# Kernel optimization log

Measured on AMD Instinct MI355X. Metric: run time of the kernel, lower is better.

## Reference

```python
import jax, jax.numpy as jnp
import numpy as np

B = 16384      # rays
H = 128        # field hidden dim


def setup_inputs() -> dict:
    key = jax.random.key(0)
    ks = jax.random.split(key, 8)
    origins = jax.random.normal(ks[0], (B, 3), dtype=jnp.float32)
    directions = jax.random.normal(ks[1], (B, 3), dtype=jnp.float32)
    directions = directions / jnp.linalg.norm(directions, axis=-1, keepdims=True)
    # Field: simple MLP 3 -> H -> H -> 4 (rgb + sigma)
    W1 = jax.random.normal(ks[2], (3, H), dtype=jnp.float32) * (1.0 / np.sqrt(3.0))
    b1 = jnp.zeros((H,), dtype=jnp.float32)
    W2 = jax.random.normal(ks[3], (H, H), dtype=jnp.float32) * (1.0 / np.sqrt(H))
    b2 = jnp.zeros((H,), dtype=jnp.float32)
    W3 = jax.random.normal(ks[4], (H, 4), dtype=jnp.float32) * (1.0 / np.sqrt(H))
    b3 = jnp.zeros((4,), dtype=jnp.float32)
    return {"origins": origins, "directions": directions,
            "W1": W1, "b1": b1, "W2": W2, "b2": b2, "W3": W3, "b3": b3,
            "near": 2, "far": 6, "num_samples": 64}


def _field(x, W1, b1, W2, b2, W3, b3):
    h = jax.nn.relu(x @ W1 + b1)
    h = jax.nn.relu(h @ W2 + b2)
    return h @ W3 + b3


def reference(origins, directions, W1, b1, W2, b2, W3, b3, near, far, num_samples):
    near = jnp.float32(near)
    far = jnp.float32(far)
    # 1. generate_samples: segment boundaries + midpoints along each ray
    depths = jnp.linspace(near, far, num_samples + 1)            # [S+1]
    midpoints = 0.5 * (depths[:-1] + depths[1:])                 # [S]
    # [B, S, 3] = origin + t * direction
    locs = origins[:, None, :] + midpoints[None, :, None] * directions[:, None, :]
    # 2. evaluate field
    f = _field(locs.reshape(-1, 3), W1, b1, W2, b2, W3, b3)
    f = f.reshape(origins.shape[0], num_samples, 4)
    # NOTE: source overwrites the sigmoid'd colors with raw outputs (faithful)
    colors = f[..., :3]                                          # [B, S, 3]
    sigma = f[..., 3]                                            # [B, S]
    # 3. alpha values
    delta = depths[1:] - depths[:-1]                             # [S]
    alphas = 1.0 - jnp.exp(-sigma * delta[None, :])              # [B, S]
    # 4. alpha compositing (black background)
    ones = jnp.ones_like(alphas[:, :1])
    transmittance = jnp.cumprod(jnp.concatenate([ones, 1.0 - alphas], axis=1), axis=1)[:, :-1]
    weights = alphas * transmittance                             # [B, S]
    radiance = jnp.sum(weights[..., None] * colors, axis=1)      # [B, 3]
    return radiance
```

## Files before the change

### kernel.cpp

```cpp
#include <hip/hip_runtime.h>


typedef _Float16 f16;
typedef __attribute__((ext_vector_type(2))) _Float16 h2v;
typedef __attribute__((ext_vector_type(8))) _Float16 half8;
typedef __attribute__((ext_vector_type(4))) float floatx4;

#define H 128
#define NS 64

static __device__ __forceinline__ h2v pkrtz(float a, float b) {
  return __builtin_bit_cast(h2v, __builtin_amdgcn_cvt_pkrtz(a, b));
}

__global__ void nerf_setup(const float* __restrict__ W2, const float* __restrict__ W3,
                           const float* __restrict__ b2,
                           f16* __restrict__ wsW2, f16* __restrict__ wsW3,
                           f16* __restrict__ wsB2) {
  int t = blockIdx.x * blockDim.x + threadIdx.x;
  if (t < 8192) {
    int j2 = t & 3, lane = (t >> 2) & 63, mt = (t >> 8) & 7, ks = t >> 11;
    int l16 = lane & 15;
    int k = ks * 32 + ((lane >> 4) * 8) + 2 * j2;
    int n = 32 * (l16 >> 2) + mt * 4 + (l16 & 3);
    wsW2[2 * t]     = (f16)W2[k * H + n];
    wsW2[2 * t + 1] = (f16)W2[(k + 1) * H + n];
  } else if (t < 9216) {
    int u = t - 8192;
    int j2 = u & 3, lane = (u >> 2) & 63, ks = u >> 8;
    int c = lane & 15;
    int k3 = 32 * (lane >> 4) + ks * 8 + 2 * j2;
    wsW3[2 * u]     = (c < 4) ? (f16)W3[k3 * 4 + c]       : (f16)0.0f;
    wsW3[2 * u + 1] = (c < 4) ? (f16)W3[(k3 + 1) * 4 + c] : (f16)0.0f;
  } else if (t < 9344) {
    int i = t - 9216;
    wsB2[i] = (f16)b2[i];
  }
}

__global__ __launch_bounds__(256, 2) void nerf_main(
    const float* __restrict__ origins, const float* __restrict__ dirs,
    const float* __restrict__ W1, const float* __restrict__ b1,
    const float* __restrict__ b3,
    const f16* __restrict__ wsW2, const f16* __restrict__ wsW3,
    const f16* __restrict__ wsB2,
    float* __restrict__ out)
{
  __shared__ __align__(16) f16   popd[4][2][H];
  __shared__ __align__(16) float f_lds[4][64][4];

  const int t = threadIdx.x;
  const int w = t >> 6, lane = t & 63, quad = lane >> 4, l16 = lane & 15;
  const float delta = 4.0f / NS;
  const int ray = blockIdx.x * 4 + w;

  {
    const float o0 = origins[ray*3], o1 = origins[ray*3+1], o2 = origins[ray*3+2];
    const float d0 = dirs[ray*3],    d1 = dirs[ray*3+1],    d2 = dirs[ray*3+2];
    const int k0 = lane * 2;
    const float2 wr0 = *(const float2*)&W1[0*H + k0];
    const float2 wr1 = *(const float2*)&W1[1*H + k0];
    const float2 wr2 = *(const float2*)&W1[2*H + k0];
    const float2 bb  = *(const float2*)&b1[k0];
    float poa = fmaf(o2, wr2.x, fmaf(o1, wr1.x, fmaf(o0, wr0.x, bb.x)));
    float pob = fmaf(o2, wr2.y, fmaf(o1, wr1.y, fmaf(o0, wr0.y, bb.y)));
    float pda = fmaf(d2, wr2.x, fmaf(d1, wr1.x, d0 * wr0.x));
    float pdb = fmaf(d2, wr2.y, fmaf(d1, wr1.y, d0 * wr0.y));
    h2v po2; po2[0] = (f16)poa; po2[1] = (f16)pob;
    h2v pd2; pd2[0] = (f16)pda; pd2[1] = (f16)pdb;
    *(h2v*)&popd[w][0][k0] = po2;
    *(h2v*)&popd[w][1][k0] = pd2;
  }

  half8 m8[4];
  #pragma unroll
  for (int tr = 0; tr < 4; ++tr)
    m8[tr] = (half8)(f16)(2.0f + (tr*16 + l16 + 0.5f) * delta);

  floatx4 acc[8][4];
  #pragma unroll
  for (int mt = 0; mt < 8; ++mt)
    #pragma unroll
    for (int tr = 0; tr < 4; ++tr) acc[mt][tr] = (floatx4)(0.0f);

  const half8* w2f = (const half8*)wsW2;
  const half8 z8 = (half8)(f16)0.0f;
  half8 awA[8], awB[8];
  #pragma unroll
  for (int mt = 0; mt < 8; ++mt) awA[mt] = w2f[mt*64 + lane];

  #pragma unroll
  for (int ks = 0; ks < 4; ++ks) {
    half8* cur = (ks & 1) ? awB : awA;
    half8* nxt = (ks & 1) ? awA : awB;
    if (ks < 3) {
      #pragma unroll
      for (int mt = 0; mt < 8; ++mt) nxt[mt] = w2f[((ks+1)*8 + mt)*64 + lane];
    }
    const half8 po8 = *(const half8*)&popd[w][0][ks*32 + quad*8];
    const half8 pd8 = *(const half8*)&popd[w][1][ks*32 + quad*8];
    #pragma unroll
    for (int tr = 0; tr < 4; ++tr) {
      half8 hb = pd8 * m8[tr] + po8;
      hb = __builtin_elementwise_max(hb, z8);
      #pragma unroll
      for (int mt = 0; mt < 8; ++mt)
        acc[mt][tr] = __builtin_amdgcn_mfma_f32_16x16x32_f16(cur[mt], hb, acc[mt][tr], 0, 0, 0);
    }
  }

  h2v bk0[8], bk1[8];
  {
    const uint2* bp = (const uint2*)wsB2;
    #pragma unroll
    for (int mt = 0; mt < 8; ++mt) {
      uint2 u = bp[quad * 8 + mt];
      bk0[mt] = __builtin_bit_cast(h2v, u.x);
      bk1[mt] = __builtin_bit_cast(h2v, u.y);
    }
  }
  const half8* w3f = (const half8*)wsW3;
  half8 w3[4];
  #pragma unroll
  for (int ks = 0; ks < 4; ++ks) w3[ks] = w3f[ks*64 + lane];

  const h2v z2 = (h2v)(f16)0.0f;
  floatx4 acc3[4];
  #pragma unroll
  for (int tr = 0; tr < 4; ++tr) {
    acc3[tr] = (floatx4)(0.0f);
    #pragma unroll
    for (int ks = 0; ks < 4; ++ks) {
      const int mt0 = 2*ks, mt1 = 2*ks + 1;
      h2v c0 = __builtin_elementwise_max((h2v)(pkrtz(acc[mt0][tr][0], acc[mt0][tr][1]) + bk0[mt0]), z2);
      h2v c1 = __builtin_elementwise_max((h2v)(pkrtz(acc[mt0][tr][2], acc[mt0][tr][3]) + bk1[mt0]), z2);
      h2v c2 = __builtin_elementwise_max((h2v)(pkrtz(acc[mt1][tr][0], acc[mt1][tr][1]) + bk0[mt1]), z2);
      h2v c3 = __builtin_elementwise_max((h2v)(pkrtz(acc[mt1][tr][2], acc[mt1][tr][3]) + bk1[mt1]), z2);
      half8 b = { c0[0], c0[1], c1[0], c1[1], c2[0], c2[1], c3[0], c3[1] };
      acc3[tr] = __builtin_amdgcn_mfma_f32_16x16x32_f16(w3[ks], b, acc3[tr], 0, 0, 0);
    }
  }

  if (quad == 0) {
    #pragma unroll
    for (int tr = 0; tr < 4; ++tr) {
      float4 fv;
      fv.x = acc3[tr][0] + b3[0];
      fv.y = acc3[tr][1] + b3[1];
      fv.z = acc3[tr][2] + b3[2];
      fv.w = acc3[tr][3] + b3[3];
      *(float4*)&f_lds[w][tr*16 + l16][0] = fv;
    }
  }

  {
    const float4 fv = *(const float4*)&f_lds[w][lane][0];
    const float sigma = fv.w;
    const float alpha = 1.0f - __expf(-sigma * delta);
    float S = sigma;
    #pragma unroll
    for (int off = 1; off < 64; off <<= 1) {
      float u = __shfl_up(S, off);
      if (lane >= off) S += u;
    }
    const float T  = __expf(-delta * (S - sigma));
    const float wt = alpha * T;
    float cr = wt * fv.x, cg = wt * fv.y, cb = wt * fv.z;
    #pragma unroll
    for (int off = 32; off > 0; off >>= 1) {
      cr += __shfl_down(cr, off);
      cg += __shfl_down(cg, off);
      cb += __shfl_down(cb, off);
    }
    if (lane == 0) {
      out[ray*3+0] = cr; out[ray*3+1] = cg; out[ray*3+2] = cb;
    }
  }
}

extern "C" void kernel_launch(void* const* d_in, const int* in_sizes, int n_in,
                              void* d_out, int out_size, void* d_ws, size_t ws_size,
                              hipStream_t stream) {
  const float* origins = (const float*)d_in[0];
  const float* dirs    = (const float*)d_in[1];
  const float* W1      = (const float*)d_in[2];
  const float* b1      = (const float*)d_in[3];
  const float* W2      = (const float*)d_in[4];
  const float* b2      = (const float*)d_in[5];
  const float* W3      = (const float*)d_in[6];
  const float* b3      = (const float*)d_in[7];
  float* out = (float*)d_out;

  f16* wsW2 = (f16*)d_ws;
  f16* wsW3 = wsW2 + 16384;
  f16* wsB2 = wsW3 + 2048;

  nerf_setup<<<37, 256, 0, stream>>>(W2, W3, b2, wsW2, wsW3, wsB2);
  nerf_main<<<16384 / 4, 256, 0, stream>>>(
      origins, dirs, W1, b1, b3, wsW2, wsW3, wsB2, out);
}
```

Before: 107.9 us.

## Split each ray across two waves to cut registers and raise occupancy

```diff
diff --git a/kernel.cpp b/kernel.cpp
--- a/kernel.cpp
+++ b/kernel.cpp
@@ -38,7 +38,7 @@
   }
 }
 
-__global__ __launch_bounds__(256, 2) void nerf_main(
+__global__ __launch_bounds__(256, 3) void nerf_main(
     const float* __restrict__ origins, const float* __restrict__ dirs,
     const float* __restrict__ W1, const float* __restrict__ b1,
     const float* __restrict__ b3,
@@ -47,12 +47,14 @@
     float* __restrict__ out)
 {
   __shared__ __align__(16) f16   popd[4][2][H];
-  __shared__ __align__(16) float f_lds[4][64][4];
+  __shared__ __align__(16) float f_lds[2][64][4];
 
   const int t = threadIdx.x;
   const int w = t >> 6, lane = t & 63, quad = lane >> 4, l16 = lane & 15;
+  const int rayw  = w >> 1;
+  const int ray   = blockIdx.x * 2 + rayw;
+  const int shalf = (w & 1) * 32;
   const float delta = 4.0f / NS;
-  const int ray = blockIdx.x * 4 + w;
 
   {
     const float o0 = origins[ray*3], o1 = origins[ray*3+1], o2 = origins[ray*3+2];
@@ -72,40 +74,34 @@
     *(h2v*)&popd[w][1][k0] = pd2;
   }
 
-  half8 m8[4];
+  half8 m8[2];
   #pragma unroll
-  for (int tr = 0; tr < 4; ++tr)
-    m8[tr] = (half8)(f16)(2.0f + (tr*16 + l16 + 0.5f) * delta);
+  for (int tr = 0; tr < 2; ++tr)
+    m8[tr] = (half8)(f16)(2.0f + (shalf + tr*16 + l16 + 0.5f) * delta);
 
-  floatx4 acc[8][4];
+  floatx4 acc[8][2];
   #pragma unroll
-  for (int mt = 0; mt < 8; ++mt)
-    #pragma unroll
-    for (int tr = 0; tr < 4; ++tr) acc[mt][tr] = (floatx4)(0.0f);
+  for (int mt = 0; mt < 8; ++mt) {
+    acc[mt][0] = (floatx4)(0.0f);
+    acc[mt][1] = (floatx4)(0.0f);
+  }
 
   const half8* w2f = (const half8*)wsW2;
   const half8 z8 = (half8)(f16)0.0f;
-  half8 awA[8], awB[8];
-  #pragma unroll
-  for (int mt = 0; mt < 8; ++mt) awA[mt] = w2f[mt*64 + lane];
-
   #pragma unroll
   for (int ks = 0; ks < 4; ++ks) {
-    half8* cur = (ks & 1) ? awB : awA;
-    half8* nxt = (ks & 1) ? awA : awB;
-    if (ks < 3) {
-      #pragma unroll
-      for (int mt = 0; mt < 8; ++mt) nxt[mt] = w2f[((ks+1)*8 + mt)*64 + lane];
-    }
+    half8 aw[8];
+    #pragma unroll
+    for (int mt = 0; mt < 8; ++mt) aw[mt] = w2f[(ks*8 + mt)*64 + lane];
     const half8 po8 = *(const half8*)&popd[w][0][ks*32 + quad*8];
     const half8 pd8 = *(const half8*)&popd[w][1][ks*32 + quad*8];
     #pragma unroll
-    for (int tr = 0; tr < 4; ++tr) {
+    for (int tr = 0; tr < 2; ++tr) {
       half8 hb = pd8 * m8[tr] + po8;
       hb = __builtin_elementwise_max(hb, z8);
       #pragma unroll
       for (int mt = 0; mt < 8; ++mt)
-        acc[mt][tr] = __builtin_amdgcn_mfma_f32_16x16x32_f16(cur[mt], hb, acc[mt][tr], 0, 0, 0);
+        acc[mt][tr] = __builtin_amdgcn_mfma_f32_16x16x32_f16(aw[mt], hb, acc[mt][tr], 0, 0, 0);
     }
   }
 
@@ -125,9 +121,9 @@
   for (int ks = 0; ks < 4; ++ks) w3[ks] = w3f[ks*64 + lane];
 
   const h2v z2 = (h2v)(f16)0.0f;
-  floatx4 acc3[4];
+  floatx4 acc3[2];
   #pragma unroll
-  for (int tr = 0; tr < 4; ++tr) {
+  for (int tr = 0; tr < 2; ++tr) {
     acc3[tr] = (floatx4)(0.0f);
     #pragma unroll
     for (int ks = 0; ks < 4; ++ks) {
@@ -143,17 +139,19 @@
 
   if (quad == 0) {
     #pragma unroll
-    for (int tr = 0; tr < 4; ++tr) {
+    for (int tr = 0; tr < 2; ++tr) {
       float4 fv;
       fv.x = acc3[tr][0] + b3[0];
       fv.y = acc3[tr][1] + b3[1];
       fv.z = acc3[tr][2] + b3[2];
       fv.w = acc3[tr][3] + b3[3];
-      *(float4*)&f_lds[w][tr*16 + l16][0] = fv;
+      *(float4*)&f_lds[rayw][shalf + tr*16 + l16][0] = fv;
     }
   }
+  __syncthreads();
 
-  {
+  if (w < 2) {
+    const int rray = blockIdx.x * 2 + w;
     const float4 fv = *(const float4*)&f_lds[w][lane][0];
     const float sigma = fv.w;
     const float alpha = 1.0f - __expf(-sigma * delta);
@@ -173,7 +171,7 @@
       cb += __shfl_down(cb, off);
     }
     if (lane == 0) {
-      out[ray*3+0] = cr; out[ray*3+1] = cg; out[ray*3+2] = cb;
+      out[rray*3+0] = cr; out[rray*3+1] = cg; out[rray*3+2] = cb;
     }
   }
 }
@@ -196,6 +194,6 @@
   f16* wsB2 = wsW3 + 2048;
 
   nerf_setup<<<37, 256, 0, stream>>>(W2, W3, b2, wsW2, wsW3, wsB2);
-  nerf_main<<<16384 / 4, 256, 0, stream>>>(
+  nerf_main<<<16384 / 2, 256, 0, stream>>>(
       origins, dirs, W1, b1, b3, wsW2, wsW3, wsB2, out);
 }
```

Measured after the change: 121.6 us. 12.7% more time.
